# Kernel optimization log

Hardware: AMD Instinct MI355X
Metric: run time of the kernel (lower is better)

Reference implementation:

```python
import jax, jax.numpy as jnp
import numpy as np


def _nn_sq_dists(query, ref):
    # query: [B, N, 3], ref: [B, M, 3]
    # squared distance via ||q||^2 + ||r||^2 - 2 q.r, min over ref points
    q2 = jnp.sum(query * query, axis=-1)            # [B, N]
    r2 = jnp.sum(ref * ref, axis=-1)                # [B, M]
    cross = jnp.einsum('bnc,bmc->bnm', query, ref)  # [B, N, M]
    d = q2[:, :, None] + r2[:, None, :] - 2.0 * cross
    d = jnp.maximum(d, 0.0)  # clamp numerical negatives (true distances >= 0)
    return jnp.min(d, axis=-1)                      # [B, N] 1-NN squared dists


def setup_inputs() -> dict:
    key = jax.random.key(0)
    k1, k2 = jax.random.split(key)
    B, C, N = 4, 3, 8192
    pc2 = jax.random.normal(k1, (B, C, N), dtype=jnp.float32)
    pc1_warped = jax.random.normal(k2, (B, C, N), dtype=jnp.float32)
    return {"pc2": pc2, "pc1_warped": pc1_warped}


def reference(pc2, pc1_warped):
    # pos1 = target['pc2'], pos2 = output['pc1_warped'], both [B, 3, N]
    pos1 = jnp.transpose(pc2, (0, 2, 1))         # [B, N, 3]
    pos2 = jnp.transpose(pc1_warped, (0, 2, 1))  # [B, N, 3]
    # pointutils.knn(1, pos1, pos2): for each pos1 point, nearest in pos2.
    nn_d = _nn_sq_dists(pos1, pos2)              # [B, N]
    per_batch = jnp.sum(nn_d, axis=1)            # sum over dim 1
    loss = per_batch.mean() + per_batch.mean()
    return loss
```

## Files before the change

kernel.cpp:

```cpp
#include <hip/hip_runtime.h>


#define NPTS 8192
#define NB   4
#define WPB  8
#define BT   (WPB * 64)
#define CPW  32

typedef float f32x16 __attribute__((ext_vector_type(16)));
typedef short bf16x8 __attribute__((ext_vector_type(8)));

static __device__ __forceinline__ unsigned int f2bf(float f) {
    unsigned int u = __float_as_uint(f);
    u += 0x7FFF + ((u >> 16) & 1);
    return u >> 16;
}
static __device__ __forceinline__ float bf2f(unsigned int s) {
    return __uint_as_float(s << 16);
}

__global__ __launch_bounds__(512) void chamfer_prep(
    const float* __restrict__ pc1w,
    uint4* __restrict__ wsA,
    float* __restrict__ out)
{
    const int g = blockIdx.x * 512 + threadIdx.x;
    if (g == 0) out[0] = 0.0f;
    const int b = g >> 13, i = g & (NPTS - 1);
    const float* refb = pc1w + b * 3 * NPTS;
    float x = refb[i], y = refb[NPTS + i], z = refb[2 * NPTS + i];
    unsigned xh = f2bf(x), yh = f2bf(y), zh = f2bf(z);
    unsigned xl = f2bf(x - bf2f(xh));
    unsigned yl = f2bf(y - bf2f(yh));
    unsigned zl = f2bf(z - bf2f(zh));
    float h = -0.5f * (x * x + y * y + z * z);
    unsigned hh = f2bf(h);
    unsigned hl = f2bf(h - bf2f(hh));
    const int c = i >> 5, l = i & 31;
    uint4* dst = wsA + (((size_t)b * 256 + c) << 6);
    dst[l]      = make_uint4(xh | (xl << 16), xh | (yh << 16),
                             yl | (yh << 16), zh | (zl << 16));
    dst[32 + l] = make_uint4(zh | (hh << 16), hl, 0u, 0u);
}

static __device__ __forceinline__ bf16x8 make_bfrag(float x, float y, float z,
                                                    int lane)
{
    unsigned xh = f2bf(x), yh = f2bf(y), zh = f2bf(z);
    unsigned xl = f2bf(x - bf2f(xh));
    unsigned yl = f2bf(y - bf2f(yh));
    unsigned zl = f2bf(z - bf2f(zh));
    uint4 bu = (lane < 32)
        ? make_uint4(xh | (xh << 16), xl | (yh << 16),
                     yh | (yl << 16), zh | (zh << 16))
        : make_uint4(zl | (0x3F80u << 16), 0x3F80u, 0u, 0u);
    return __builtin_bit_cast(bf16x8, bu);
}

static __device__ __forceinline__ void proc_chunk(
    uint4 av, bf16x8 bq0, bf16x8 bq1, const f32x16& zero,
    float& rma0, float& rma1, float& rma2, float& rma3,
    float& rmb0, float& rmb1, float& rmb2, float& rmb3)
{
    bf16x8 aa = __builtin_bit_cast(bf16x8, av);
    f32x16 d0 = __builtin_amdgcn_mfma_f32_32x32x16_bf16(aa, bq0, zero, 0, 0, 0);
    f32x16 d1 = __builtin_amdgcn_mfma_f32_32x32x16_bf16(aa, bq1, zero, 0, 0, 0);
    rma0 = fmaxf(rma0, fmaxf(d0[0],  d0[1]));
    rma0 = fmaxf(rma0, fmaxf(d0[2],  d0[3]));
    rma1 = fmaxf(rma1, fmaxf(d0[4],  d0[5]));
    rma1 = fmaxf(rma1, fmaxf(d0[6],  d0[7]));
    rma2 = fmaxf(rma2, fmaxf(d0[8],  d0[9]));
    rma2 = fmaxf(rma2, fmaxf(d0[10], d0[11]));
    rma3 = fmaxf(rma3, fmaxf(d0[12], d0[13]));
    rma3 = fmaxf(rma3, fmaxf(d0[14], d0[15]));
    rmb0 = fmaxf(rmb0, fmaxf(d1[0],  d1[1]));
    rmb0 = fmaxf(rmb0, fmaxf(d1[2],  d1[3]));
    rmb1 = fmaxf(rmb1, fmaxf(d1[4],  d1[5]));
    rmb1 = fmaxf(rmb1, fmaxf(d1[6],  d1[7]));
    rmb2 = fmaxf(rmb2, fmaxf(d1[8],  d1[9]));
    rmb2 = fmaxf(rmb2, fmaxf(d1[10], d1[11]));
    rmb3 = fmaxf(rmb3, fmaxf(d1[12], d1[13]));
    rmb3 = fmaxf(rmb3, fmaxf(d1[14], d1[15]));
}

__global__ __launch_bounds__(BT, 4) void chamfer_main(
    const float* __restrict__ pc2,
    const uint4* __restrict__ wsA,
    float* __restrict__ out)
{
    __shared__ float red[WPB][64];
    const int tid  = threadIdx.x;
    const int wave = tid >> 6;
    const int lane = tid & 63;
    const int b    = blockIdx.y;
    const int qc0  = blockIdx.x * 2;

    const float* qb = pc2 + b * 3 * NPTS;
    const int qn0 = qc0 * 32 + (lane & 31);
    const int qn1 = qn0 + 32;
    float x0 = qb[qn0], y0 = qb[NPTS + qn0], z0 = qb[2 * NPTS + qn0];
    float x1 = qb[qn1], y1 = qb[NPTS + qn1], z1 = qb[2 * NPTS + qn1];
    bf16x8 bq0 = make_bfrag(x0, y0, z0, lane);
    bf16x8 bq1 = make_bfrag(x1, y1, z1, lane);

    f32x16 zero;
#pragma unroll
    for (int i = 0; i < 16; ++i) zero[i] = 0.0f;

    float rma0 = -3e38f, rma1 = -3e38f, rma2 = -3e38f, rma3 = -3e38f;
    float rmb0 = -3e38f, rmb1 = -3e38f, rmb2 = -3e38f, rmb3 = -3e38f;

    const uint4* src = wsA + (((size_t)b * 256 + wave * CPW) << 6);

    uint4 av = src[lane];
#pragma unroll 4
    for (int c = 0; c < CPW; ++c) {
        uint4 acur = av;
        if (c + 1 < CPW)
            av = src[((c + 1) << 6) + lane];
        proc_chunk(acur, bq0, bq1, zero, rma0, rma1, rma2, rma3,
                   rmb0, rmb1, rmb2, rmb3);
    }

    float rma = fmaxf(fmaxf(rma0, rma1), fmaxf(rma2, rma3));
    float rmb = fmaxf(fmaxf(rmb0, rmb1), fmaxf(rmb2, rmb3));
    rma = fmaxf(rma, __shfl_xor(rma, 32, 64));
    rmb = fmaxf(rmb, __shfl_xor(rmb, 32, 64));
    if (lane < 32) {
        red[wave][lane]      = rma;
        red[wave][32 + lane] = rmb;
    }
    __syncthreads();

    if (tid < 64) {
        float smax = red[0][tid];
#pragma unroll
        for (int w = 1; w < WPB; ++w) smax = fmaxf(smax, red[w][tid]);
        const int n = qc0 * 32 + tid;
        float qx = qb[n], qy = qb[NPTS + n], qz = qb[2 * NPTS + n];
        float d = fmaxf(qx * qx + qy * qy + qz * qz - 2.0f * smax, 0.0f);
#pragma unroll
        for (int off = 32; off > 0; off >>= 1)
            d += __shfl_down(d, off, 64);
        if (tid == 0)
            atomicAdd(out, d * (2.0f / NB));
    }
}

extern "C" void kernel_launch(void* const* d_in, const int* in_sizes, int n_in,
                              void* d_out, int out_size, void* d_ws, size_t ws_size,
                              hipStream_t stream) {
    const float* pc2  = (const float*)d_in[0];
    const float* pc1w = (const float*)d_in[1];
    float* out = (float*)d_out;
    uint4* wsA = (uint4*)d_ws;

    chamfer_prep<<<NB * NPTS / 512, 512, 0, stream>>>(pc1w, wsA, out);
    dim3 g(128, NB);
    chamfer_main<<<g, BT, 0, stream>>>(pc2, wsA, out);
}
```

Measured before the change: 76.06 us.

## Fuse reference bf16 split-packing into main kernel, drop prep kernel

Removes the separate prep kernel that packed reference points into bf16 hi/lo MFMA fragments in workspace. The main kernel now reads raw float coordinates and builds the A fragments inline each chunk, with a memset replacing the prep kernel's zeroing of the output. This saves one kernel launch and the workspace round trip. In exchange, the conversion work is repeated by every block (128x redundancy per batch) and the loop unroll is reduced to 1.

```diff
diff --git a/kernel.cpp b/kernel.cpp
--- a/kernel.cpp
+++ b/kernel.cpp
@@ -17,30 +17,6 @@
 }
 static __device__ __forceinline__ float bf2f(unsigned int s) {
     return __uint_as_float(s << 16);
-}
-
-__global__ __launch_bounds__(512) void chamfer_prep(
-    const float* __restrict__ pc1w,
-    uint4* __restrict__ wsA,
-    float* __restrict__ out)
-{
-    const int g = blockIdx.x * 512 + threadIdx.x;
-    if (g == 0) out[0] = 0.0f;
-    const int b = g >> 13, i = g & (NPTS - 1);
-    const float* refb = pc1w + b * 3 * NPTS;
-    float x = refb[i], y = refb[NPTS + i], z = refb[2 * NPTS + i];
-    unsigned xh = f2bf(x), yh = f2bf(y), zh = f2bf(z);
-    unsigned xl = f2bf(x - bf2f(xh));
-    unsigned yl = f2bf(y - bf2f(yh));
-    unsigned zl = f2bf(z - bf2f(zh));
-    float h = -0.5f * (x * x + y * y + z * z);
-    unsigned hh = f2bf(h);
-    unsigned hl = f2bf(h - bf2f(hh));
-    const int c = i >> 5, l = i & 31;
-    uint4* dst = wsA + (((size_t)b * 256 + c) << 6);
-    dst[l]      = make_uint4(xh | (xl << 16), xh | (yh << 16),
-                             yl | (yh << 16), zh | (zl << 16));
-    dst[32 + l] = make_uint4(zh | (hh << 16), hl, 0u, 0u);
 }
 
 static __device__ __forceinline__ bf16x8 make_bfrag(float x, float y, float z,
@@ -83,9 +59,9 @@
     rmb3 = fmaxf(rmb3, fmaxf(d1[14], d1[15]));
 }
 
-__global__ __launch_bounds__(BT, 4) void chamfer_main(
+__global__ __launch_bounds__(BT, 4) void chamfer_fused(
     const float* __restrict__ pc2,
-    const uint4* __restrict__ wsA,
+    const float* __restrict__ pc1w,
     float* __restrict__ out)
 {
     __shared__ float red[WPB][64];
@@ -110,15 +86,32 @@
     float rma0 = -3e38f, rma1 = -3e38f, rma2 = -3e38f, rma3 = -3e38f;
     float rmb0 = -3e38f, rmb1 = -3e38f, rmb2 = -3e38f, rmb3 = -3e38f;
 
-    const uint4* src = wsA + (((size_t)b * 256 + wave * CPW) << 6);
+    const float* refb = pc1w + b * 3 * NPTS;
+    const int rbase = wave * (CPW * 32) + (lane & 31);
 
-    uint4 av = src[lane];
-#pragma unroll 4
+    float rx = refb[rbase], ry = refb[NPTS + rbase], rz = refb[2 * NPTS + rbase];
+#pragma unroll 1
     for (int c = 0; c < CPW; ++c) {
-        uint4 acur = av;
-        if (c + 1 < CPW)
-            av = src[((c + 1) << 6) + lane];
-        proc_chunk(acur, bq0, bq1, zero, rma0, rma1, rma2, rma3,
+        float cx = rx, cy = ry, cz = rz;
+        if (c + 1 < CPW) {
+            const int i = rbase + (c + 1) * 32;
+            rx = refb[i]; ry = refb[NPTS + i]; rz = refb[2 * NPTS + i];
+        }
+        unsigned xh = f2bf(cx), yh = f2bf(cy), zh = f2bf(cz);
+        uint4 av;
+        if (lane < 32) {
+            unsigned xl = f2bf(cx - bf2f(xh));
+            unsigned yl = f2bf(cy - bf2f(yh));
+            unsigned zl = f2bf(cz - bf2f(zh));
+            av = make_uint4(xh | (xl << 16), xh | (yh << 16),
+                            yl | (yh << 16), zh | (zl << 16));
+        } else {
+            float h = -0.5f * (cx * cx + cy * cy + cz * cz);
+            unsigned hh = f2bf(h);
+            unsigned hl = f2bf(h - bf2f(hh));
+            av = make_uint4(zh | (hh << 16), hl, 0u, 0u);
+        }
+        proc_chunk(av, bq0, bq1, zero, rma0, rma1, rma2, rma3,
                    rmb0, rmb1, rmb2, rmb3);
     }
 
@@ -153,9 +146,10 @@
     const float* pc2  = (const float*)d_in[0];
     const float* pc1w = (const float*)d_in[1];
     float* out = (float*)d_out;
-    uint4* wsA = (uint4*)d_ws;
+    (void)d_ws; (void)ws_size;
 
-    chamfer_prep<<<NB * NPTS / 512, 512, 0, stream>>>(pc1w, wsA, out);
+    hipMemsetAsync(out, 0, sizeof(float), stream);
+
     dim3 g(128, NB);
-    chamfer_main<<<g, BT, 0, stream>>>(pc2, wsA, out);
+    chamfer_fused<<<g, BT, 0, stream>>>(pc2, pc1w, out);
 }
```

New measurement: 86.03 us. 13.1% more time.

## Stage reference chunks in LDS per block and reduce partial maxima separately

Applied to the files above, without the earlier changes.

The separate prep kernel is removed. Each block now converts a 1024-point slice of the reference cloud into the split-bf16 MFMA layout directly in shared memory, and all 8 waves share that tile, each working on its own 64 queries. Per-slice row maxima go to a global partial buffer, and a new reduce kernel takes the max over the 8 slices, computes distances and sums them. This trades the global-memory operand loads in the hot loop for LDS reads. The cost is that each reference slice is converted redundantly in every query-group block, plus an extra partial-buffer write and read.

```diff
diff --git a/kernel.cpp b/kernel.cpp
--- a/kernel.cpp
+++ b/kernel.cpp
@@ -3,9 +3,9 @@
 
 #define NPTS 8192
 #define NB   4
-#define WPB  8
-#define BT   (WPB * 64)
-#define CPW  32
+#define RRN  8
+#define QGN  16
+#define BT   512
 
 typedef float f32x16 __attribute__((ext_vector_type(16)));
 typedef short bf16x8 __attribute__((ext_vector_type(8)));
@@ -17,30 +17,6 @@
 }
 static __device__ __forceinline__ float bf2f(unsigned int s) {
     return __uint_as_float(s << 16);
-}
-
-__global__ __launch_bounds__(512) void chamfer_prep(
-    const float* __restrict__ pc1w,
-    uint4* __restrict__ wsA,
-    float* __restrict__ out)
-{
-    const int g = blockIdx.x * 512 + threadIdx.x;
-    if (g == 0) out[0] = 0.0f;
-    const int b = g >> 13, i = g & (NPTS - 1);
-    const float* refb = pc1w + b * 3 * NPTS;
-    float x = refb[i], y = refb[NPTS + i], z = refb[2 * NPTS + i];
-    unsigned xh = f2bf(x), yh = f2bf(y), zh = f2bf(z);
-    unsigned xl = f2bf(x - bf2f(xh));
-    unsigned yl = f2bf(y - bf2f(yh));
-    unsigned zl = f2bf(z - bf2f(zh));
-    float h = -0.5f * (x * x + y * y + z * z);
-    unsigned hh = f2bf(h);
-    unsigned hl = f2bf(h - bf2f(hh));
-    const int c = i >> 5, l = i & 31;
-    uint4* dst = wsA + (((size_t)b * 256 + c) << 6);
-    dst[l]      = make_uint4(xh | (xl << 16), xh | (yh << 16),
-                             yl | (yh << 16), zh | (zl << 16));
-    dst[32 + l] = make_uint4(zh | (hh << 16), hl, 0u, 0u);
 }
 
 static __device__ __forceinline__ bf16x8 make_bfrag(float x, float y, float z,
@@ -85,16 +61,40 @@
 
 __global__ __launch_bounds__(BT, 4) void chamfer_main(
     const float* __restrict__ pc2,
-    const uint4* __restrict__ wsA,
+    const float* __restrict__ pc1w,
+    float* __restrict__ partial,
     float* __restrict__ out)
 {
-    __shared__ float red[WPB][64];
+    __shared__ uint4 slds[32 * 64];
     const int tid  = threadIdx.x;
     const int wave = tid >> 6;
     const int lane = tid & 63;
-    const int b    = blockIdx.y;
-    const int qc0  = blockIdx.x * 2;
+    const int b    = blockIdx.z;
+    const int rr   = blockIdx.y;
+    const int qg   = blockIdx.x;
 
+    if (qg == 0 && rr == 0 && b == 0 && tid == 0) out[0] = 0.0f;
+
+    const float* refb = pc1w + b * 3 * NPTS + rr * 1024;
+#pragma unroll
+    for (int j = 0; j < 2; ++j) {
+        int i = tid + j * BT;
+        float x = refb[i], y = refb[NPTS + i], z = refb[2 * NPTS + i];
+        unsigned xh = f2bf(x), yh = f2bf(y), zh = f2bf(z);
+        unsigned xl = f2bf(x - bf2f(xh));
+        unsigned yl = f2bf(y - bf2f(yh));
+        unsigned zl = f2bf(z - bf2f(zh));
+        float h = -0.5f * (x * x + y * y + z * z);
+        unsigned hh = f2bf(h);
+        unsigned hl = f2bf(h - bf2f(hh));
+        int c = i >> 5, l32 = i & 31;
+        slds[c * 64 + l32] =
+            make_uint4(xh | (xl << 16), xh | (yh << 16),
+                       yl | (yh << 16), zh | (zl << 16));
+        slds[c * 64 + 32 + l32] = make_uint4(zh | (hh << 16), hl, 0u, 0u);
+    }
+
+    const int qc0 = qg * 16 + wave * 2;
     const float* qb = pc2 + b * 3 * NPTS;
     const int qn0 = qc0 * 32 + (lane & 31);
     const int qn1 = qn0 + 32;
@@ -110,14 +110,14 @@
     float rma0 = -3e38f, rma1 = -3e38f, rma2 = -3e38f, rma3 = -3e38f;
     float rmb0 = -3e38f, rmb1 = -3e38f, rmb2 = -3e38f, rmb3 = -3e38f;
 
-    const uint4* src = wsA + (((size_t)b * 256 + wave * CPW) << 6);
+    __syncthreads();
 
-    uint4 av = src[lane];
+    uint4 av = slds[lane];
 #pragma unroll 4
-    for (int c = 0; c < CPW; ++c) {
+    for (int c = 0; c < 32; ++c) {
         uint4 acur = av;
-        if (c + 1 < CPW)
-            av = src[((c + 1) << 6) + lane];
+        if (c + 1 < 32)
+            av = slds[(c + 1) * 64 + lane];
         proc_chunk(acur, bq0, bq1, zero, rma0, rma1, rma2, rma3,
                    rmb0, rmb1, rmb2, rmb3);
     }
@@ -126,24 +126,44 @@
     float rmb = fmaxf(fmaxf(rmb0, rmb1), fmaxf(rmb2, rmb3));
     rma = fmaxf(rma, __shfl_xor(rma, 32, 64));
     rmb = fmaxf(rmb, __shfl_xor(rmb, 32, 64));
+    float* pb = partial + ((size_t)b * RRN + rr) * NPTS + qc0 * 32;
     if (lane < 32) {
-        red[wave][lane]      = rma;
-        red[wave][32 + lane] = rmb;
+        pb[lane]      = rma;
+        pb[32 + lane] = rmb;
     }
+}
+
+__global__ __launch_bounds__(512) void chamfer_reduce(
+    const float* __restrict__ pc2,
+    const float* __restrict__ partial,
+    float* __restrict__ out)
+{
+    const int g = blockIdx.x * 512 + threadIdx.x;
+    const int b = g >> 13, n = g & 8191;
+    float smax = -3e38f;
+#pragma unroll
+    for (int c = 0; c < RRN; ++c)
+        smax = fmaxf(smax, partial[((size_t)b * RRN + c) * NPTS + n]);
+
+    const float* qb = pc2 + b * 3 * NPTS;
+    float qx = qb[n], qy = qb[NPTS + n], qz = qb[2 * NPTS + n];
+    float q2 = qx * qx + qy * qy + qz * qz;
+    float d = fmaxf(q2 - 2.0f * smax, 0.0f);
+
+#pragma unroll
+    for (int off = 32; off > 0; off >>= 1)
+        d += __shfl_down(d, off, 64);
+
+    __shared__ float wsum[8];
+    const int lane = threadIdx.x & 63;
+    const int wid  = threadIdx.x >> 6;
+    if (lane == 0) wsum[wid] = d;
     __syncthreads();
-
-    if (tid < 64) {
-        float smax = red[0][tid];
+    if (threadIdx.x == 0) {
+        float s = 0.0f;
 #pragma unroll
-        for (int w = 1; w < WPB; ++w) smax = fmaxf(smax, red[w][tid]);
-        const int n = qc0 * 32 + tid;
-        float qx = qb[n], qy = qb[NPTS + n], qz = qb[2 * NPTS + n];
-        float d = fmaxf(qx * qx + qy * qy + qz * qz - 2.0f * smax, 0.0f);
-#pragma unroll
-        for (int off = 32; off > 0; off >>= 1)
-            d += __shfl_down(d, off, 64);
-        if (tid == 0)
-            atomicAdd(out, d * (2.0f / NB));
+        for (int w = 0; w < 8; ++w) s += wsum[w];
+        atomicAdd(out, s * (2.0f / NB));
     }
 }
 
@@ -153,9 +173,9 @@
     const float* pc2  = (const float*)d_in[0];
     const float* pc1w = (const float*)d_in[1];
     float* out = (float*)d_out;
-    uint4* wsA = (uint4*)d_ws;
+    float* partial = (float*)d_ws;
 
-    chamfer_prep<<<NB * NPTS / 512, 512, 0, stream>>>(pc1w, wsA, out);
-    dim3 g(128, NB);
-    chamfer_main<<<g, BT, 0, stream>>>(pc2, wsA, out);
+    dim3 g1(QGN, RRN, NB);
+    chamfer_main<<<g1, BT, 0, stream>>>(pc2, pc1w, partial, out);
+    chamfer_reduce<<<NB * NPTS / 512, 512, 0, stream>>>(pc2, partial, out);
 }
```

Result: faster. 73.51 us (median of 2 runs) (-3.4%).
